# Kernel tuning notes

Hardware: AMD Instinct MI355X
Metric: run time of the kernel (lower is better)

Reference implementation:

```python
import jax, jax.numpy as jnp
import numpy as np

NUM_HEADS = 16
D_MODEL = 1024
D_QKV = 64


def _xavier(key, shape):
    # xavier normal over last two dims (fan_in = D_MODEL, fan_out = D_QKV)
    std = float(np.sqrt(2.0 / (shape[-2] + shape[-1])))
    return jax.random.normal(key, shape, dtype=jnp.float32) * std


def setup_inputs() -> dict:
    key = jax.random.key(0)
    ks = jax.random.split(key, 9)
    B, L = 4, 2048
    q = jax.random.normal(ks[0], (B, L, D_MODEL), dtype=jnp.float32)
    k = jax.random.normal(ks[1], (B, L, D_MODEL), dtype=jnp.float32)
    v = jax.random.normal(ks[2], (B, L, D_MODEL), dtype=jnp.float32)
    mask = jax.random.randint(ks[3], (B, L, L), 0, 2, dtype=jnp.int32)
    Wq = _xavier(ks[4], (NUM_HEADS, D_MODEL, D_QKV))
    Wk = _xavier(ks[5], (NUM_HEADS, D_MODEL, D_QKV))
    Wv = _xavier(ks[6], (NUM_HEADS, D_MODEL, D_QKV))
    lim = float(1.0 / np.sqrt(D_MODEL))
    Wo_w = jax.random.uniform(ks[7], (D_MODEL, D_MODEL), minval=-lim, maxval=lim, dtype=jnp.float32)
    Wo_b = jax.random.uniform(ks[8], (D_MODEL,), minval=-lim, maxval=lim, dtype=jnp.float32)
    return {"q": q, "k": k, "v": v, "mask": mask,
            "Wq": Wq, "Wk": Wk, "Wv": Wv, "Wo_w": Wo_w, "Wo_b": Wo_b}


def reference(q, k, v, mask, Wq, Wk, Wv, Wo_w, Wo_b):
    B, L, _ = q.shape
    query = jnp.einsum('blm,nmd->bnld', q, Wq)   # [B,H,L,Dq]
    key_ = jnp.einsum('blm,nmd->bnld', k, Wk)
    value = jnp.einsum('blm,nmd->bnld', v, Wv)
    scores = jnp.einsum('bnld,bnmd->bnlm', query, key_) / jnp.sqrt(
        jnp.asarray(D_QKV, dtype=query.dtype))          # [B,H,L,L]
    scores = jnp.where(mask[:, None, :, :] == 0, jnp.asarray(-1e9, scores.dtype), scores)
    attn = jax.nn.softmax(scores, axis=-1)
    out = jnp.einsum('bnlm,bnmd->bnld', attn, value)     # [B,H,L,Dq]
    out = out.transpose(0, 2, 1, 3).reshape(B, L, D_MODEL)
    return out @ Wo_w.T + Wo_b
```

## Files before the change

### kernel.cpp

```cpp
#include <hip/hip_runtime.h>
#include <stdint.h>

typedef __bf16 bf16;
typedef __bf16 bf16x8 __attribute__((ext_vector_type(8)));
typedef float  f32x4  __attribute__((ext_vector_type(4)));
typedef uint32_t u32;
typedef uint64_t u64;

#define SCALE_L2E 0.18033688011112042f

__device__ __forceinline__ void gld_lds16(const void* gsrc, void* ldst) {
  __builtin_amdgcn_global_load_lds(
      (const __attribute__((address_space(1))) void*)gsrc,
      (__attribute__((address_space(3))) void*)ldst, 16, 0, 0);
}


__global__ void cvt3(const float* __restrict__ q, const float* __restrict__ k,
                     const float* __restrict__ v, bf16* __restrict__ out) {
  const float* in = (blockIdx.z == 0) ? q : (blockIdx.z == 1) ? k : v;
  bf16* o = out + (size_t)blockIdx.z * 8388608;
  int stride = gridDim.x * blockDim.x;
  for (int i = blockIdx.x * blockDim.x + threadIdx.x; i < 1048576; i += stride) {
    const float4* p = (const float4*)(in + (size_t)i * 8);
    float4 a = p[0], b = p[1];
    bf16x8 vv;
    vv[0]=(bf16)a.x; vv[1]=(bf16)a.y; vv[2]=(bf16)a.z; vv[3]=(bf16)a.w;
    vv[4]=(bf16)b.x; vv[5]=(bf16)b.y; vv[6]=(bf16)b.z; vv[7]=(bf16)b.w;
    *(bf16x8*)(o + (size_t)i * 8) = vv;
  }
}

__global__ void pack_w(const float* __restrict__ Wq, const float* __restrict__ Wk,
                       const float* __restrict__ Wv, const float* __restrict__ Wo,
                       bf16* __restrict__ Wt) {
  int s = blockIdx.z;
  int tid = blockIdx.x * blockDim.x + threadIdx.x;
  int n = tid >> 7, kb = tid & 127;
  const float* W = (s == 0) ? Wq : (s == 1) ? Wk : (s == 2) ? Wv : Wo;
  bf16x8 v;
  if (s < 3) {
#pragma unroll
    for (int j = 0; j < 8; ++j)
      v[j] = (bf16)W[((n >> 6) << 16) + (kb * 8 + j) * 64 + (n & 63)];
  } else {
    const float4* p = (const float4*)&W[n * 1024 + kb * 8];
    float4 a = p[0], b = p[1];
    v[0]=(bf16)a.x; v[1]=(bf16)a.y; v[2]=(bf16)a.z; v[3]=(bf16)a.w;
    v[4]=(bf16)b.x; v[5]=(bf16)b.y; v[6]=(bf16)b.z; v[7]=(bf16)b.w;
  }
  *(bf16x8*)&Wt[(size_t)s * 1048576 + (size_t)n * 1024 + kb * 8] = v;
}

__global__ void pack_mask(const int* __restrict__ mask, u32* __restrict__ mbits, int total) {
  int stride = gridDim.x * blockDim.x;
  for (int idx = blockIdx.x * blockDim.x + threadIdx.x; idx < total; idx += stride) {
    int v = mask[idx];
    u64 bal = __ballot(v != 0);
    if ((threadIdx.x & 63) == 0)
      *(u64*)&mbits[idx >> 5] = bal;
  }
}

template<int EPI>
__global__ __launch_bounds__(256, 2)
void gemm_bt(const bf16* __restrict__ A, const bf16* __restrict__ Bt,
             void* __restrict__ Cout, void* __restrict__ Cout2,
             const float* __restrict__ bias,
             size_t a_bstride, size_t b_bstride, float cscale) {
  const int gx = gridDim.x;
  int lin = blockIdx.y * gx + blockIdx.x;
  int nwg = gx * gridDim.y;
  int swz = (lin & 7) * (nwg >> 3) + (lin >> 3);
  int bx = swz % gx, by = swz / gx;
  const int bz = blockIdx.z;
  A  += a_bstride * bz;
  Bt += b_bstride * bz;
  const int row0 = by * 128, col0 = bx * 128;
  bool isK = false;
  if (EPI == 0 && row0 >= 8192) { isK = true; Bt += 1048576; }

  __shared__ bf16 sA[2][4096];
  __shared__ bf16 sB[2][4096];

  const int lane = threadIdx.x & 63, w = threadIdx.x >> 6;
  const int c = lane & 15, g = lane >> 4;
  const int wr = w >> 1, wc = w & 1;

  const int u0 = w * 128 + lane;
  const int rs0 = u0 >> 2, ps0 = u0 & 3;
  const int rs1 = (u0 + 64) >> 2, ps1 = (u0 + 64) & 3;
  const bf16* Ap = A + (size_t)row0 * 1024;
  const bf16* Bp = Bt + (size_t)col0 * 1024;
  const bf16* As0 = Ap + (size_t)rs0 * 1024 + ps0 * 8;
  const bf16* As1 = Ap + (size_t)rs1 * 1024 + ps1 * 8;
  const bf16* Bs0 = Bp + (size_t)rs0 * 1024 + ps0 * 8;
  const bf16* Bs1 = Bp + (size_t)rs1 * 1024 + ps1 * 8;

  f32x4 acc[4][4] = {};

  gld_lds16(As0, (char*)&sA[0][0] + (w * 2) * 1024);
  gld_lds16(As1, (char*)&sA[0][0] + (w * 2 + 1) * 1024);
  gld_lds16(Bs0, (char*)&sB[0][0] + (w * 2) * 1024);
  gld_lds16(Bs1, (char*)&sB[0][0] + (w * 2 + 1) * 1024);

  for (int k0 = 0; k0 < 1024; k0 += 32) {
    __syncthreads();
    int cb = (k0 >> 5) & 1, nb = cb ^ 1;
    if (k0 < 992) {
      gld_lds16(As0 + k0 + 32, (char*)&sA[nb][0] + (w * 2) * 1024);
      gld_lds16(As1 + k0 + 32, (char*)&sA[nb][0] + (w * 2 + 1) * 1024);
      gld_lds16(Bs0 + k0 + 32, (char*)&sB[nb][0] + (w * 2) * 1024);
      gld_lds16(Bs1 + k0 + 32, (char*)&sB[nb][0] + (w * 2 + 1) * 1024);
    }

    bf16x8 af[4], bfr[4];
#pragma unroll
    for (int m = 0; m < 4; ++m)
      af[m] = *(const bf16x8*)&sA[cb][(wr * 64 + m * 16 + c) * 32 + g * 8];
#pragma unroll
    for (int n = 0; n < 4; ++n)
      bfr[n] = *(const bf16x8*)&sB[cb][(wc * 64 + n * 16 + c) * 32 + g * 8];
#pragma unroll
    for (int m = 0; m < 4; ++m)
#pragma unroll
      for (int n = 0; n < 4; ++n)
        acc[m][n] = __builtin_amdgcn_mfma_f32_16x16x32_bf16(af[m], bfr[n], acc[m][n], 0, 0, 0);
  }

  float csc = (EPI == 0 && isK) ? 1.0f : cscale;
#pragma unroll
  for (int m = 0; m < 4; ++m) {
    int row_base = row0 + wr * 64 + m * 16 + g * 4;
#pragma unroll
    for (int n = 0; n < 4; ++n) {
      int col = col0 + wc * 64 + n * 16 + c;
#pragma unroll
      for (int r = 0; r < 4; ++r) {
        int row = row_base + r;
        float val = acc[m][n][r];
        if (EPI == 0) {
          int rl = row & 8191;
          int b = rl >> 11, l = rl & 2047, h = col >> 6, d = col & 63;
          bf16* dst = isK ? (bf16*)Cout2 : (bf16*)Cout;
          dst[(((size_t)(b * 16 + h) * 2048 + l) << 6) + d] = (bf16)(val * csc);
        } else if (EPI == 1) {
          ((bf16*)Cout)[((size_t)(bz * 1024 + row)) * 2048 + col] = (bf16)val;
        } else {
          ((float*)Cout)[(size_t)row * 1024 + col] = val + bias[col];
        }
      }
    }
  }
}

__global__ __launch_bounds__(256, 3)
void attn_fwd(const bf16* __restrict__ Qp, const bf16* __restrict__ Kp,
              const bf16* __restrict__ Vt, const u32* __restrict__ mbits,
              bf16* __restrict__ X) {
  int lin = blockIdx.y * 16 + blockIdx.x;
  int swz = (lin & 7) * 128 + (lin >> 3);
  int qt = swz & 15, bh = swz >> 4;
  int b = bh >> 4, h = bh & 15;
  int q0 = qt * 128;

  const int tid = threadIdx.x;
  const int lane = tid & 63, w = tid >> 6;
  const int c = lane & 15, g = lane >> 4;

  __shared__ char smem[49152];
  char* sKV = smem;
  char* sPw = smem + 32768 + w * 4096;

  const int c7 = c & 7;
  const int y0 = (g ^ c7) << 4;
  const int y1 = ((4 + g) ^ c7) << 4;
  const int ko0 = c * 128 + y0;
  const int ko1 = c * 128 + y1;
  const int vo0 = 8192 + c * 128 + y0;
  const int vo1 = 8192 + c * 128 + y1;
  const char* paddr0 = sPw + c * 128 + y0;
  const char* paddr1 = sPw + c * 128 + y1;
  char* pw[4];
#pragma unroll
  for (int nk = 0; nk < 4; ++nk)
    pw[nk] = sPw + c * 128 + ((g & 1) * 8) + (((nk * 2 + (g >> 1)) ^ c7) << 4);

  const int r0 = tid >> 3, bb0 = tid & 7;
  const int r1 = (256 + tid) >> 3, bb1 = tid & 7;
  const int dK0 = r0 * 128 + ((bb0 ^ (r0 & 7)) << 4);
  const int dK1 = r1 * 128 + ((bb1 ^ (r1 & 7)) << 4);
  const int dV0 = 8192 + dK0;
  const int dV1 = 8192 + dK1;
  const bf16* gK0 = Kp + (size_t)bh * 131072 + r0 * 64 + bb0 * 8;
  const bf16* gK1 = Kp + (size_t)bh * 131072 + r1 * 64 + bb1 * 8;
  const bf16* gV0 = Vt + ((size_t)(b * 1024 + h * 64 + r0)) * 2048 + bb0 * 8;
  const bf16* gV1 = Vt + ((size_t)(b * 1024 + h * 64 + r1)) * 2048 + bb1 * 8;

  const bf16* Qbase = Qp + ((size_t)bh * 2048) * 64;
  bf16x8 qf[2][2];
#pragma unroll
  for (int nq = 0; nq < 2; ++nq) {
    int qg = q0 + w * 32 + nq * 16 + c;
#pragma unroll
    for (int kk = 0; kk < 2; ++kk)
      qf[nq][kk] = *(const bf16x8*)&Qbase[(size_t)qg * 64 + kk * 32 + g * 8];
  }

  const u64* Mrow0 = (const u64*)(mbits + ((size_t)b * 2048 + (q0 + w * 32 + c)) * 64);
  const u64* Mrow1 = (const u64*)(mbits + ((size_t)b * 2048 + (q0 + w * 32 + 16 + c)) * 64);

  f32x4 oacc[4][2] = {};
  float lrun0 = 0.f, lrun1 = 0.f;

  {
    uint4 kr0 = *(const uint4*)gK0, kr1 = *(const uint4*)gK1;
    uint4 vr0 = *(const uint4*)gV0, vr1 = *(const uint4*)gV1;
    *(uint4*)(sKV + dK0) = kr0; *(uint4*)(sKV + dK1) = kr1;
    *(uint4*)(sKV + dV0) = vr0; *(uint4*)(sKV + dV1) = vr1;
  }
  u64 mw0 = Mrow0[0], mw1 = Mrow1[0];

  for (int t = 0; t < 32; ++t) {
    __syncthreads();
    const char* kbuf = sKV + ((t & 1) << 14);

    uint4 kr0, kr1, vr0, vr1;
    u64 mn0 = 0, mn1 = 0;
    if (t < 31) {
      kr0 = *(const uint4*)(gK0 + (size_t)(t + 1) * 4096);
      kr1 = *(const uint4*)(gK1 + (size_t)(t + 1) * 4096);
      vr0 = *(const uint4*)(gV0 + (size_t)(t + 1) * 64);
      vr1 = *(const uint4*)(gV1 + (size_t)(t + 1) * 64);
      mn0 = Mrow0[t + 1];
      mn1 = Mrow1[t + 1];
    }

    f32x4 st[4][2] = {};
#pragma unroll
    for (int nk = 0; nk < 4; ++nk) {
      bf16x8 kfa = *(const bf16x8*)(kbuf + ko0 + nk * 2048);
      st[nk][0] = __builtin_amdgcn_mfma_f32_16x16x32_bf16(kfa, qf[0][0], st[nk][0], 0, 0, 0);
      st[nk][1] = __builtin_amdgcn_mfma_f32_16x16x32_bf16(kfa, qf[1][0], st[nk][1], 0, 0, 0);
      bf16x8 kfb = *(const bf16x8*)(kbuf + ko1 + nk * 2048);
      st[nk][0] = __builtin_amdgcn_mfma_f32_16x16x32_bf16(kfb, qf[0][1], st[nk][0], 0, 0, 0);
      st[nk][1] = __builtin_amdgcn_mfma_f32_16x16x32_bf16(kfb, qf[1][1], st[nk][1], 0, 0, 0);
    }

#pragma unroll
    for (int nq = 0; nq < 2; ++nq) {
      u64 ms = (nq ? mw1 : mw0) >> (4 * g);
      u32 ma = (u32)ms;
      u32 mb = (u32)(ms >> 32);
      float ls = 0.f;
#pragma unroll
      for (int nk = 0; nk < 4; ++nk) {
        u32 msel = (nk < 2) ? ma : mb;
        const int bs = (nk & 1) * 16;
#pragma unroll
        for (int tt = 0; tt < 2; ++tt) {
          float e0 = __builtin_amdgcn_exp2f(st[nk][nq][tt * 2]);
          float e1 = __builtin_amdgcn_exp2f(st[nk][nq][tt * 2 + 1]);
          e0 = (msel & (1u << (bs + tt * 2)))     ? e0 : 0.f;
          e1 = (msel & (1u << (bs + tt * 2 + 1))) ? e1 : 0.f;
          ls += e0;
          ls += e1;
          union { bf16 h2[2]; u32 uu; } pk;
          pk.h2[0] = (bf16)e0; pk.h2[1] = (bf16)e1;
          *(u32*)(pw[nk] + nq * 2048 + tt * 4) = pk.uu;
        }
      }
      if (nq) lrun1 += ls; else lrun0 += ls;
    }

#pragma unroll
    for (int kk = 0; kk < 2; ++kk) {
      const char* pa = kk ? paddr1 : paddr0;
      const int vo = kk ? vo1 : vo0;
      bf16x8 pf0 = *(const bf16x8*)(pa);
      bf16x8 pf1 = *(const bf16x8*)(pa + 2048);
#pragma unroll
      for (int md = 0; md < 4; ++md) {
        bf16x8 vf = *(const bf16x8*)(kbuf + vo + md * 2048);
        oacc[md][0] = __builtin_amdgcn_mfma_f32_16x16x32_bf16(vf, pf0, oacc[md][0], 0, 0, 0);
        oacc[md][1] = __builtin_amdgcn_mfma_f32_16x16x32_bf16(vf, pf1, oacc[md][1], 0, 0, 0);
      }
    }

    if (t < 31) {
      char* nbuf = sKV + (((t + 1) & 1) << 14);
      *(uint4*)(nbuf + dK0) = kr0; *(uint4*)(nbuf + dK1) = kr1;
      *(uint4*)(nbuf + dV0) = vr0; *(uint4*)(nbuf + dV1) = vr1;
    }
    mw0 = mn0; mw1 = mn1;
  }

  lrun0 += __shfl_xor(lrun0, 16); lrun0 += __shfl_xor(lrun0, 32);
  lrun1 += __shfl_xor(lrun1, 16); lrun1 += __shfl_xor(lrun1, 32);
  float inv0 = 1.f / lrun0;
  float inv1 = 1.f / lrun1;

  __syncthreads();
  char* Xl = smem;
#pragma unroll
  for (int nq = 0; nq < 2; ++nq) {
    float inv = nq ? inv1 : inv0;
    int ql = w * 32 + nq * 16 + c;
#pragma unroll
    for (int md = 0; md < 4; ++md)
#pragma unroll
      for (int r = 0; r < 4; ++r) {
        int d = md * 16 + g * 4 + r;
        int blk = d >> 3, off = d & 7;
        *(bf16*)(Xl + ql * 128 + ((blk ^ (ql & 7)) << 4) + off * 2) =
            (bf16)(oacc[md][nq][r] * inv);
      }
  }
  __syncthreads();
#pragma unroll
  for (int i = 0; i < 4; ++i) {
    int u = i * 256 + tid;
    int row = u >> 3, blk = u & 7;
    uint4 xv = *(const uint4*)(Xl + row * 128 + ((blk ^ (row & 7)) << 4));
    *(uint4*)&X[(size_t)(b * 2048 + q0 + row) * 1024 + h * 64 + blk * 8] = xv;
  }
}


extern "C" void kernel_launch(void* const* d_in, const int* in_sizes, int n_in,
                              void* d_out, int out_size, void* d_ws, size_t ws_size,
                              hipStream_t stream) {
  const float* q    = (const float*)d_in[0];
  const float* k    = (const float*)d_in[1];
  const float* v    = (const float*)d_in[2];
  const int*   mask = (const int*)d_in[3];
  const float* Wq   = (const float*)d_in[4];
  const float* Wk   = (const float*)d_in[5];
  const float* Wv   = (const float*)d_in[6];
  const float* Wo   = (const float*)d_in[7];
  const float* Wb   = (const float*)d_in[8];

  char* ws = (char*)d_ws;
  bf16* qb = (bf16*)(ws + 0);
  bf16* kb = (bf16*)(ws + 16777216);
  bf16* vb = (bf16*)(ws + 33554432);
  bf16* Wt = (bf16*)(ws + 50331648);
  bf16* Qp = (bf16*)(ws + 58720256);
  bf16* Kp = (bf16*)(ws + 75497472);
  bf16* Vt = (bf16*)(ws + 92274688);
  bf16* Xb = (bf16*)(ws + 109051904);
  u32*  mb = (u32*) (ws + 125829120);

  cvt3<<<dim3(512, 1, 3), 256, 0, stream>>>(q, k, v, qb);
  pack_w<<<dim3(512, 1, 4), 256, 0, stream>>>(Wq, Wk, Wv, Wo, Wt);
  pack_mask<<<2048, 256, 0, stream>>>(mask, mb, 16777216);

  gemm_bt<0><<<dim3(8, 128, 1), 256, 0, stream>>>(qb, Wt, Qp, Kp, nullptr, 0, 0, SCALE_L2E);
  gemm_bt<1><<<dim3(16, 8, 4), 256, 0, stream>>>(Wt + 2097152, vb, Vt, nullptr, nullptr, 0, 2097152, 1.0f);

  attn_fwd<<<dim3(16, 64, 1), 256, 0, stream>>>(Qp, Kp, Vt, mb, Xb);

  gemm_bt<2><<<dim3(8, 64, 1), 256, 0, stream>>>(Xb, Wt + 3145728, (float*)d_out, nullptr, Wb, 0, 0, 1.0f);
}
```

Measured before the change: 263.9 us.

## Software-pipeline attention loop: compute next QK^T scores during current softmax/PV

Restructures the attention main loop so the QK^T MFMAs for tile t+1 are issued before the exp/mask/PV work of tile t. Global prefetch is moved two tiles ahead and a double-buffered score register set is used. The row-sum is now computed with an MFMA against a ones vector instead of scalar adds and shuffles, and s_setprio wraps the MFMA sections. The extra live registers lead to lowering launch bounds occupancy from 3 to 2, and an extra barrier is added per iteration.

Measured after the change: 272.8 us. 3.4% more time.

```diff
diff --git a/kernel.cpp b/kernel.cpp
--- a/kernel.cpp
+++ b/kernel.cpp
@@ -154,7 +154,85 @@
   }
 }
 
-__global__ __launch_bounds__(256, 3)
+
+#define ATTN_ITER(t, PAR, SP, SC)                                              \
+  {                                                                            \
+    const char* kbC = sKV + ((PAR) << 14);                                     \
+    const char* kbN = sKV + (((PAR) ^ 1) << 14);                               \
+    if ((t) < 31) {                                                            \
+      __builtin_amdgcn_s_setprio(1);                                           \
+      _Pragma("unroll")                                                        \
+      for (int nk = 0; nk < 4; ++nk) {                                         \
+        bf16x8 kfa = *(const bf16x8*)(kbN + ko0 + nk * 2048);                  \
+        bf16x8 kfb = *(const bf16x8*)(kbN + ko1 + nk * 2048);                  \
+        f32x4 z = {0.f, 0.f, 0.f, 0.f};                                        \
+        SC[nk][0] = __builtin_amdgcn_mfma_f32_16x16x32_bf16(kfb, qf[0][1],     \
+            __builtin_amdgcn_mfma_f32_16x16x32_bf16(kfa, qf[0][0], z, 0,0,0),  \
+            0, 0, 0);                                                          \
+        SC[nk][1] = __builtin_amdgcn_mfma_f32_16x16x32_bf16(kfb, qf[1][1],     \
+            __builtin_amdgcn_mfma_f32_16x16x32_bf16(kfa, qf[1][0], z, 0,0,0),  \
+            0, 0, 0);                                                          \
+      }                                                                        \
+      __builtin_amdgcn_s_setprio(0);                                           \
+    }                                                                          \
+    if ((t) < 30) {                                                            \
+      kr0 = *(const uint4*)(gK0 + (size_t)((t) + 2) * 4096);                   \
+      kr1 = *(const uint4*)(gK1 + (size_t)((t) + 2) * 4096);                   \
+      vr0 = *(const uint4*)(gV0 + (size_t)((t) + 2) * 64);                     \
+      vr1 = *(const uint4*)(gV1 + (size_t)((t) + 2) * 64);                     \
+      mwi0 = Mrow0[(t) + 2];                                                   \
+      mwi1 = Mrow1[(t) + 2];                                                   \
+    }                                                                          \
+    _Pragma("unroll")                                                          \
+    for (int nq = 0; nq < 2; ++nq) {                                           \
+      u64 ms = (nq ? mwc1 : mwc0) >> (4 * g);                                  \
+      u32 ma = (u32)ms, mb2 = (u32)(ms >> 32);                                 \
+      _Pragma("unroll")                                                        \
+      for (int nk = 0; nk < 4; ++nk) {                                         \
+        u32 msel = (nk < 2) ? ma : mb2;                                        \
+        const int bs = (nk & 1) * 16;                                          \
+        float e0 = __builtin_amdgcn_exp2f(SP[nk][nq][0]);                      \
+        float e1 = __builtin_amdgcn_exp2f(SP[nk][nq][1]);                      \
+        float e2 = __builtin_amdgcn_exp2f(SP[nk][nq][2]);                      \
+        float e3 = __builtin_amdgcn_exp2f(SP[nk][nq][3]);                      \
+        e0 = (msel & (1u << (bs + 0))) ? e0 : 0.f;                             \
+        e1 = (msel & (1u << (bs + 1))) ? e1 : 0.f;                             \
+        e2 = (msel & (1u << (bs + 2))) ? e2 : 0.f;                             \
+        e3 = (msel & (1u << (bs + 3))) ? e3 : 0.f;                             \
+        union { bf16 h[4]; uint2 d; } pk;                                      \
+        pk.h[0] = (bf16)e0; pk.h[1] = (bf16)e1;                                \
+        pk.h[2] = (bf16)e2; pk.h[3] = (bf16)e3;                                \
+        *(uint2*)(pw[nk] + nq * 2048) = pk.d;                                  \
+      }                                                                        \
+    }                                                                          \
+    __builtin_amdgcn_s_setprio(1);                                             \
+    _Pragma("unroll")                                                          \
+    for (int kk = 0; kk < 2; ++kk) {                                           \
+      const char* pa = kk ? paddr1 : paddr0;                                   \
+      const int vo = kk ? vo1 : vo0;                                           \
+      bf16x8 pf0 = *(const bf16x8*)(pa);                                       \
+      bf16x8 pf1 = *(const bf16x8*)(pa + 2048);                                \
+      dacc[0] = __builtin_amdgcn_mfma_f32_16x16x32_bf16(onesv, pf0, dacc[0], 0, 0, 0); \
+      dacc[1] = __builtin_amdgcn_mfma_f32_16x16x32_bf16(onesv, pf1, dacc[1], 0, 0, 0); \
+      _Pragma("unroll")                                                        \
+      for (int md = 0; md < 4; ++md) {                                         \
+        bf16x8 vf = *(const bf16x8*)(kbC + vo + md * 2048);                    \
+        oacc[md][0] = __builtin_amdgcn_mfma_f32_16x16x32_bf16(vf, pf0, oacc[md][0], 0, 0, 0); \
+        oacc[md][1] = __builtin_amdgcn_mfma_f32_16x16x32_bf16(vf, pf1, oacc[md][1], 0, 0, 0); \
+      }                                                                        \
+    }                                                                          \
+    __builtin_amdgcn_s_setprio(0);                                             \
+    __syncthreads();                                                           \
+    if ((t) < 30) {                                                            \
+      char* nb = sKV + ((PAR) << 14);                                          \
+      *(uint4*)(nb + dK0o) = kr0; *(uint4*)(nb + dK1o) = kr1;                  \
+      *(uint4*)(nb + dV0o) = vr0; *(uint4*)(nb + dV1o) = vr1;                  \
+    }                                                                          \
+    mwc0 = mwn0; mwc1 = mwn1; mwn0 = mwi0; mwn1 = mwi1;                        \
+    __syncthreads();                                                           \
+  }
+
+__global__ __launch_bounds__(256, 2)
 void attn_fwd(const bf16* __restrict__ Qp, const bf16* __restrict__ Kp,
               const bf16* __restrict__ Vt, const u32* __restrict__ mbits,
               bf16* __restrict__ X) {
@@ -188,10 +266,10 @@
 
   const int r0 = tid >> 3, bb0 = tid & 7;
   const int r1 = (256 + tid) >> 3, bb1 = tid & 7;
-  const int dK0 = r0 * 128 + ((bb0 ^ (r0 & 7)) << 4);
-  const int dK1 = r1 * 128 + ((bb1 ^ (r1 & 7)) << 4);
-  const int dV0 = 8192 + dK0;
-  const int dV1 = 8192 + dK1;
+  const int dK0o = r0 * 128 + ((bb0 ^ (r0 & 7)) << 4);
+  const int dK1o = r1 * 128 + ((bb1 ^ (r1 & 7)) << 4);
+  const int dV0o = 8192 + dK0o;
+  const int dV1o = 8192 + dK1o;
   const bf16* gK0 = Kp + (size_t)bh * 131072 + r0 * 64 + bb0 * 8;
   const bf16* gK1 = Kp + (size_t)bh * 131072 + r1 * 64 + bb1 * 8;
   const bf16* gV0 = Vt + ((size_t)(b * 1024 + h * 64 + r0)) * 2048 + bb0 * 8;
@@ -207,100 +285,55 @@
       qf[nq][kk] = *(const bf16x8*)&Qbase[(size_t)qg * 64 + kk * 32 + g * 8];
   }
 
+  bf16x8 onesv;
+#pragma unroll
+  for (int i = 0; i < 8; ++i) onesv[i] = (bf16)1.0f;
+
   const u64* Mrow0 = (const u64*)(mbits + ((size_t)b * 2048 + (q0 + w * 32 + c)) * 64);
   const u64* Mrow1 = (const u64*)(mbits + ((size_t)b * 2048 + (q0 + w * 32 + 16 + c)) * 64);
 
   f32x4 oacc[4][2] = {};
-  float lrun0 = 0.f, lrun1 = 0.f;
+  f32x4 dacc[2] = {};
+  f32x4 sa[4][2], sb[4][2];
+  uint4 kr0, kr1, vr0, vr1;
+  u64 mwc0, mwc1, mwn0, mwn1, mwi0 = 0, mwi1 = 0;
 
   {
-    uint4 kr0 = *(const uint4*)gK0, kr1 = *(const uint4*)gK1;
-    uint4 vr0 = *(const uint4*)gV0, vr1 = *(const uint4*)gV1;
-    *(uint4*)(sKV + dK0) = kr0; *(uint4*)(sKV + dK1) = kr1;
-    *(uint4*)(sKV + dV0) = vr0; *(uint4*)(sKV + dV1) = vr1;
-  }
-  u64 mw0 = Mrow0[0], mw1 = Mrow1[0];
-
-  for (int t = 0; t < 32; ++t) {
-    __syncthreads();
-    const char* kbuf = sKV + ((t & 1) << 14);
-
-    uint4 kr0, kr1, vr0, vr1;
-    u64 mn0 = 0, mn1 = 0;
-    if (t < 31) {
-      kr0 = *(const uint4*)(gK0 + (size_t)(t + 1) * 4096);
-      kr1 = *(const uint4*)(gK1 + (size_t)(t + 1) * 4096);
-      vr0 = *(const uint4*)(gV0 + (size_t)(t + 1) * 64);
-      vr1 = *(const uint4*)(gV1 + (size_t)(t + 1) * 64);
-      mn0 = Mrow0[t + 1];
-      mn1 = Mrow1[t + 1];
-    }
-
-    f32x4 st[4][2] = {};
-#pragma unroll
-    for (int nk = 0; nk < 4; ++nk) {
-      bf16x8 kfa = *(const bf16x8*)(kbuf + ko0 + nk * 2048);
-      st[nk][0] = __builtin_amdgcn_mfma_f32_16x16x32_bf16(kfa, qf[0][0], st[nk][0], 0, 0, 0);
-      st[nk][1] = __builtin_amdgcn_mfma_f32_16x16x32_bf16(kfa, qf[1][0], st[nk][1], 0, 0, 0);
-      bf16x8 kfb = *(const bf16x8*)(kbuf + ko1 + nk * 2048);
-      st[nk][0] = __builtin_amdgcn_mfma_f32_16x16x32_bf16(kfb, qf[0][1], st[nk][0], 0, 0, 0);
-      st[nk][1] = __builtin_amdgcn_mfma_f32_16x16x32_bf16(kfb, qf[1][1], st[nk][1], 0, 0, 0);
-    }
-
-#pragma unroll
-    for (int nq = 0; nq < 2; ++nq) {
-      u64 ms = (nq ? mw1 : mw0) >> (4 * g);
-      u32 ma = (u32)ms;
-      u32 mb = (u32)(ms >> 32);
-      float ls = 0.f;
-#pragma unroll
-      for (int nk = 0; nk < 4; ++nk) {
-        u32 msel = (nk < 2) ? ma : mb;
-        const int bs = (nk & 1) * 16;
-#pragma unroll
-        for (int tt = 0; tt < 2; ++tt) {
-          float e0 = __builtin_amdgcn_exp2f(st[nk][nq][tt * 2]);
-          float e1 = __builtin_amdgcn_exp2f(st[nk][nq][tt * 2 + 1]);
-          e0 = (msel & (1u << (bs + tt * 2)))     ? e0 : 0.f;
-          e1 = (msel & (1u << (bs + tt * 2 + 1))) ? e1 : 0.f;
-          ls += e0;
-          ls += e1;
-          union { bf16 h2[2]; u32 uu; } pk;
-          pk.h2[0] = (bf16)e0; pk.h2[1] = (bf16)e1;
-          *(u32*)(pw[nk] + nq * 2048 + tt * 4) = pk.uu;
-        }
-      }
-      if (nq) lrun1 += ls; else lrun0 += ls;
-    }
-
-#pragma unroll
-    for (int kk = 0; kk < 2; ++kk) {
-      const char* pa = kk ? paddr1 : paddr0;
-      const int vo = kk ? vo1 : vo0;
-      bf16x8 pf0 = *(const bf16x8*)(pa);
-      bf16x8 pf1 = *(const bf16x8*)(pa + 2048);
-#pragma unroll
-      for (int md = 0; md < 4; ++md) {
-        bf16x8 vf = *(const bf16x8*)(kbuf + vo + md * 2048);
-        oacc[md][0] = __builtin_amdgcn_mfma_f32_16x16x32_bf16(vf, pf0, oacc[md][0], 0, 0, 0);
-        oacc[md][1] = __builtin_amdgcn_mfma_f32_16x16x32_bf16(vf, pf1, oacc[md][1], 0, 0, 0);
-      }
-    }
-
-    if (t < 31) {
-      char* nbuf = sKV + (((t + 1) & 1) << 14);
-      *(uint4*)(nbuf + dK0) = kr0; *(uint4*)(nbuf + dK1) = kr1;
-      *(uint4*)(nbuf + dV0) = vr0; *(uint4*)(nbuf + dV1) = vr1;
-    }
-    mw0 = mn0; mw1 = mn1;
-  }
-
-  lrun0 += __shfl_xor(lrun0, 16); lrun0 += __shfl_xor(lrun0, 32);
-  lrun1 += __shfl_xor(lrun1, 16); lrun1 += __shfl_xor(lrun1, 32);
-  float inv0 = 1.f / lrun0;
-  float inv1 = 1.f / lrun1;
-
+    uint4 a0 = *(const uint4*)gK0, a1 = *(const uint4*)gK1;
+    uint4 b0 = *(const uint4*)gV0, b1 = *(const uint4*)gV1;
+    uint4 c0 = *(const uint4*)(gK0 + 4096), c1 = *(const uint4*)(gK1 + 4096);
+    uint4 d0 = *(const uint4*)(gV0 + 64),   d1 = *(const uint4*)(gV1 + 64);
+    *(uint4*)(sKV + dK0o) = a0; *(uint4*)(sKV + dK1o) = a1;
+    *(uint4*)(sKV + dV0o) = b0; *(uint4*)(sKV + dV1o) = b1;
+    *(uint4*)(sKV + 16384 + dK0o) = c0; *(uint4*)(sKV + 16384 + dK1o) = c1;
+    *(uint4*)(sKV + 16384 + dV0o) = d0; *(uint4*)(sKV + 16384 + dV1o) = d1;
+  }
+  mwc0 = Mrow0[0]; mwc1 = Mrow1[0];
+  mwn0 = Mrow0[1]; mwn1 = Mrow1[1];
   __syncthreads();
+
+  __builtin_amdgcn_s_setprio(1);
+#pragma unroll
+  for (int nk = 0; nk < 4; ++nk) {
+    bf16x8 kfa = *(const bf16x8*)(sKV + ko0 + nk * 2048);
+    bf16x8 kfb = *(const bf16x8*)(sKV + ko1 + nk * 2048);
+    f32x4 z = {0.f, 0.f, 0.f, 0.f};
+    sa[nk][0] = __builtin_amdgcn_mfma_f32_16x16x32_bf16(kfb, qf[0][1],
+        __builtin_amdgcn_mfma_f32_16x16x32_bf16(kfa, qf[0][0], z, 0, 0, 0), 0, 0, 0);
+    sa[nk][1] = __builtin_amdgcn_mfma_f32_16x16x32_bf16(kfb, qf[1][1],
+        __builtin_amdgcn_mfma_f32_16x16x32_bf16(kfa, qf[1][0], z, 0, 0, 0), 0, 0, 0);
+  }
+  __builtin_amdgcn_s_setprio(0);
+
+  for (int t2 = 0; t2 < 16; ++t2) {
+    int ta = 2 * t2, tb = 2 * t2 + 1;
+    ATTN_ITER(ta, 0, sa, sb);
+    ATTN_ITER(tb, 1, sb, sa);
+  }
+
+  float inv0 = 1.f / dacc[0][0];
+  float inv1 = 1.f / dacc[1][0];
+
   char* Xl = smem;
 #pragma unroll
   for (int nq = 0; nq < 2; ++nq) {
```
